# Optimization experiments

Hardware: AMD Instinct MI355X
Metric: run time of the kernel (lower is better)

The kernel has to match this reference:

```python
import jax, jax.numpy as jnp
import numpy as np

M = 15
WIN = 5  # tension detector window_size
SIGMA = 0.1
_ZETA = np.array([14.134725, 21.02204, 25.010858, 30.424876, 32.935062,
                  37.586178, 40.91872, 43.327073, 48.005151, 49.773832,
                  52.970321, 56.446248, 59.347044, 60.831779, 65.112544], dtype=np.float32)
GAMMAS = jnp.asarray(_ZETA)                       # [M]
PHI = jnp.asarray(np.exp(-SIGMA * np.abs(_ZETA)).astype(np.float32))  # [M]

B, S, I, H = 256, 512, 256, 512


def setup_inputs() -> dict:
    key = jax.random.key(0)
    ks = jax.random.split(key, 12)
    s_i = 1.0 / np.sqrt(I)
    s_h = 1.0 / np.sqrt(H)
    return {
        "x": jax.random.normal(ks[0], (B, S, I), dtype=jnp.float32),
        # LSTMCell params (PyTorch layout: gates i,f,g,o)
        "W_ih": jax.random.normal(ks[1], (4 * H, I), dtype=jnp.float32) * s_i,
        "W_hh": jax.random.normal(ks[2], (4 * H, H), dtype=jnp.float32) * s_h,
        "b_ih": jax.random.normal(ks[3], (4 * H,), dtype=jnp.float32) * s_h,
        "b_hh": jax.random.normal(ks[4], (4 * H,), dtype=jnp.float32) * s_h,
        # spectrum analyzer input_proj: Linear(I -> 2M)
        "W_proj": jax.random.normal(ks[5], (2 * M, I), dtype=jnp.float32) * s_i,
        "b_proj": jax.random.normal(ks[6], (2 * M,), dtype=jnp.float32) * s_i,
        # tension detector change_detector: Linear(2H->H), ReLU, Linear(H->1), Sigmoid
        "W_t1": jax.random.normal(ks[7], (H, 2 * H), dtype=jnp.float32) * (1.0 / np.sqrt(2 * H)),
        "b_t1": jax.random.normal(ks[8], (H,), dtype=jnp.float32) * s_h,
        "W_t2": jax.random.normal(ks[9], (1, H), dtype=jnp.float32) * s_h,
        "b_t2": jax.random.normal(ks[10], (1,), dtype=jnp.float32) * s_h,
        # zeta memory gate_combiner: Linear(2 -> 1)
        "W_g": jax.random.normal(ks[11], (1, 2), dtype=jnp.float32) * 0.5,
        "b_g": jnp.zeros((1,), dtype=jnp.float32),
    }


def _forward(x, W_ih, W_hh, b_ih, b_hh, W_proj, b_proj, W_t1, b_t1, W_t2, b_t2, W_g, b_g):
    batch = x.shape[0]
    seq_len = x.shape[1]
    hid = W_hh.shape[1]

    h0 = jnp.zeros((batch, hid), dtype=x.dtype)
    c0 = jnp.zeros((batch, hid), dtype=x.dtype)
    hist0 = jnp.zeros((batch, WIN, hid), dtype=x.dtype)

    def step(carry, inp):
        h, c, hist = carry
        x_t, t = inp                      # x_t: [B, I], t: scalar int
        tf = t.astype(x.dtype)

        # LSTMCell (produces h_new, c_new)
        gates = x_t @ W_ih.T + b_ih + h @ W_hh.T + b_hh   # [B, 4H]
        gi, gf, gg, go = jnp.split(gates, 4, axis=1)
        c_new = jax.nn.sigmoid(gf) * c + jax.nn.sigmoid(gi) * jnp.tanh(gg)
        h_new = jax.nn.sigmoid(go) * jnp.tanh(c_new)

        # ZetaSpectrumAnalyzer on x_t
        proj = x_t @ W_proj.T + b_proj                     # [B, 2M]
        cos_coeffs, sin_coeffs = proj[:, :M], proj[:, M:]
        zc = jnp.cos(GAMMAS * tf)                          # [M]
        zs = jnp.sin(GAMMAS * tf)
        cos_corr = jnp.sum(cos_coeffs * zc * PHI, axis=1)
        sin_corr = jnp.sum(sin_coeffs * zs * PHI, axis=1)
        resonance = jax.nn.sigmoid(jnp.sqrt(cos_corr**2 + sin_corr**2 + 1e-8) - 0.5)[:, None]  # [B,1]

        # TensionMarkerDetector on OLD h (history stores detached old h)
        hist = hist.at[:, t % WIN].set(jax.lax.stop_gradient(h))
        h_mean = hist.mean(axis=1)                         # [B, H]
        comp = jnp.concatenate([h, h_mean], axis=1)        # [B, 2H]
        tension = jax.nn.sigmoid(jax.nn.relu(comp @ W_t1.T + b_t1) @ W_t2.T + b_t2)  # [B,1]
        tension = jnp.where(t < 2, jnp.zeros_like(tension), tension)

        # ZetaMemoryGated on OLD h
        zeta_weight = jnp.sum(PHI * jnp.cos(GAMMAS * tf)) / M  # scalar
        m_raw = zeta_weight * h                                # [B, H]
        gate_in = jnp.concatenate([resonance, tension], axis=1)  # [B, 2]
        gate = jax.nn.sigmoid(gate_in @ W_g.T + b_g)             # [B, 1]
        h_out = h_new + gate * m_raw

        return (h_out, c_new, hist), h_out

    xs = (jnp.swapaxes(x, 0, 1), jnp.arange(seq_len, dtype=jnp.int32))
    (h_n, c_n, _), ys = jax.lax.scan(step, (h0, c0, hist0), xs)
    output = jnp.swapaxes(ys, 0, 1)        # [B, S, H]
    return output, h_n[None], c_n[None]


def reference(x, W_ih, W_hh, b_ih, b_hh, W_proj, b_proj, W_t1, b_t1, W_t2, b_t2, W_g, b_g):
    return _forward(x, W_ih, W_hh, b_ih, b_hh, W_proj, b_proj, W_t1, b_t1, W_t2, b_t2, W_g, b_g)
```

## Files before the change

### kernel.cpp

```cpp
#include <hip/hip_runtime.h>

typedef _Float16 f16;
typedef _Float16 f16x8 __attribute__((ext_vector_type(8)));
typedef float f32x4 __attribute__((ext_vector_type(4)));
typedef float f32x2 __attribute__((ext_vector_type(2)));
typedef unsigned long long u64;

#define DEVFN static __device__ __forceinline__

#define NBLK 256

#define OFF_WCAT 0ULL
#define OFF_WT1A (OFF_WCAT + 2048ULL*768*2)
#define OFF_WT1B (OFF_WT1A + 512ULL*512*2)
#define OFF_HB0  (OFF_WT1B + 512ULL*512*2)
#define OFF_HB1  (OFF_HB0  + 256ULL*512*2)
#define OFF_XB0  (OFF_HB1  + 256ULL*512*2)
#define OFF_XB1  (OFF_XB0  + 256ULL*256*2)
#define OFF_XB2  (OFF_XB1  + 256ULL*256*2)
#define OFF_BSUM (OFF_XB2  + 256ULL*256*2)
#define OFF_U    (OFF_BSUM + 2048ULL*4)
#define OFF_V    (OFF_U    + 512ULL*256*4)
#define OFF_CU   (OFF_V    + 512ULL*256*4)
#define OFF_CV   (OFF_CU   + 512ULL*4)
#define OFF_ZETA (OFF_CV   + 512ULL*4)
#define OFF_RES  (OFF_ZETA + 512ULL*4)
#define OFF_TENSP (OFF_RES + 512ULL*256*4)
#define OFF_SLOT (OFF_TENSP + 16384ULL*4)

__constant__ float CGAM[15] = {14.134725f, 21.02204f, 25.010858f, 30.424876f, 32.935062f,
  37.586178f, 40.91872f, 43.327073f, 48.005151f, 49.773832f, 52.970321f,
  56.446248f, 59.347044f, 60.831779f, 65.112544f};

DEVFN float sigf(float v) { return 1.f / (1.f + __expf(-v)); }
DEVFN float tanh_(float v) {
  v = fminf(fmaxf(v, -15.f), 15.f);
  float e = __expf(2.f * v);
  return (e - 1.f) / (e + 1.f);
}

DEVFN float ald_f32(const float* p) {
  unsigned v = __hip_atomic_load((const unsigned*)p, __ATOMIC_RELAXED, __HIP_MEMORY_SCOPE_AGENT);
  union { unsigned u; float f; } c; c.u = v; return c.f;
}
DEVFN void ast_f32(float* p, float v) {
  union { float f; unsigned u; } c; c.f = v;
  __hip_atomic_store((unsigned*)p, c.u, __ATOMIC_RELAXED, __HIP_MEMORY_SCOPE_AGENT);
}
DEVFN u64 ald_u64(const void* p) {
  return __hip_atomic_load((const u64*)p, __ATOMIC_RELAXED, __HIP_MEMORY_SCOPE_AGENT);
}
DEVFN void ast_u32(void* p, unsigned v) {
  __hip_atomic_store((unsigned*)p, v, __ATOMIC_RELAXED, __HIP_MEMORY_SCOPE_AGENT);
}

DEVFN void post(unsigned* slot, unsigned v) {
  asm volatile("s_waitcnt vmcnt(0)" ::: "memory");
  __syncthreads();
  if (threadIdx.x == 0)
    __hip_atomic_store(slot, v, __ATOMIC_RELAXED, __HIP_MEMORY_SCOPE_AGENT);
}
DEVFN void wait_line(const unsigned* line, unsigned target) {
  if (threadIdx.x < 64) {
    const unsigned* pp = line + (threadIdx.x & 31);
    long sp = 0;
    for (;;) {
      unsigned v = __hip_atomic_load(pp, __ATOMIC_RELAXED, __HIP_MEMORY_SCOPE_AGENT);
      if (__all(v >= target)) break;
      __builtin_amdgcn_s_sleep(1);
      if (++sp > (1L << 21)) break;
    }
  }
  __syncthreads();
}

__global__ void k_init(const float* __restrict__ x, const float* __restrict__ Wih,
                       const float* __restrict__ Whh, const float* __restrict__ bih,
                       const float* __restrict__ bhh, const float* __restrict__ Wt1f,
                       char* __restrict__ ws) {
  f16* Wcat = (f16*)(ws + OFF_WCAT);
  f16* WhmA = (f16*)(ws + OFF_WT1A);
  f16* WmB  = (f16*)(ws + OFF_WT1B);
  f16* hb0  = (f16*)(ws + OFF_HB0);
  f16* xb0  = (f16*)(ws + OFF_XB0);
  f16* xb1  = (f16*)(ws + OFF_XB1);
  float* bsum = (float*)(ws + OFF_BSUM);
  float* tensP = (float*)(ws + OFF_TENSP);
  unsigned* slots = (unsigned*)(ws + OFF_SLOT);
  int gtid = blockIdx.x * blockDim.x + threadIdx.x;
  int nth = gridDim.x * blockDim.x;
  for (int i = gtid; i < 2048 * 768; i += nth) {
    int n = i / 768, k = i - n * 768;
    float w = (k < 256) ? Wih[n * 256 + k] : Whh[n * 512 + (k - 256)];
    Wcat[i] = (f16)w;
  }
  for (int i = gtid; i < 512 * 512; i += nth) {
    int n = i >> 9, k = i & 511;
    float wh = Wt1f[n * 1024 + k];
    float wm = Wt1f[n * 1024 + 512 + k] * 0.2f;
    WhmA[i] = (f16)(wh + wm);
    WmB[i]  = (f16)wm;
  }
  for (int i = gtid; i < 2048; i += nth) bsum[i] = bih[i] + bhh[i];
  for (int i = gtid; i < 256 * 512; i += nth) hb0[i] = (f16)0.f;
  for (int i = gtid; i < 256 * 256; i += nth) {
    int b = i >> 8, k = i & 255;
    xb0[i] = (f16)x[(size_t)b * 131072 + k];
    xb1[i] = (f16)x[(size_t)b * 131072 + 256 + k];
  }
  for (int i = gtid; i < 16384; i += nth) tensP[i] = 0.f;
  for (int i = gtid; i < 8 * 64; i += nth) slots[i] = 0u;
}

__global__ void k_tables(const float* __restrict__ Wproj, const float* __restrict__ bproj,
                         char* __restrict__ ws) {
  float* u    = (float*)(ws + OFF_U);
  float* v    = (float*)(ws + OFF_V);
  float* cu   = (float*)(ws + OFF_CU);
  float* cv   = (float*)(ws + OFF_CV);
  float* zeta = (float*)(ws + OFF_ZETA);
  int t = blockIdx.x;
  int k = threadIdx.x;
  float tf = (float)t;
  float cg[15], sg[15], ph[15];
  #pragma unroll
  for (int m = 0; m < 15; ++m) {
    float ang = CGAM[m] * tf;
    cg[m] = cosf(ang);
    sg[m] = sinf(ang);
    ph[m] = (float)exp(-0.1 * (double)CGAM[m]);
  }
  float uu = 0.f, vv = 0.f;
  #pragma unroll
  for (int m = 0; m < 15; ++m) {
    uu += Wproj[m * 256 + k] * cg[m] * ph[m];
    vv += Wproj[(15 + m) * 256 + k] * sg[m] * ph[m];
  }
  u[t * 256 + k] = uu;
  v[t * 256 + k] = vv;
  if (k == 0) {
    float a = 0.f, b2 = 0.f, z = 0.f;
    #pragma unroll
    for (int m = 0; m < 15; ++m) {
      a  += bproj[m] * cg[m] * ph[m];
      b2 += bproj[15 + m] * sg[m] * ph[m];
      z  += ph[m] * cg[m];
    }
    cu[t] = a; cv[t] = b2; zeta[t] = z / 15.f;
  }
}

__global__ void k_res(const float* __restrict__ x, char* __restrict__ ws) {
  const float* u  = (const float*)(ws + OFF_U);
  const float* v  = (const float*)(ws + OFF_V);
  const float* cu = (const float*)(ws + OFF_CU);
  const float* cv = (const float*)(ws + OFF_CV);
  float* resb     = (float*)(ws + OFF_RES);
  int wid = blockIdx.x * 4 + (threadIdx.x >> 6);
  int l = threadIdx.x & 63;
  int b = wid >> 9, t = wid & 511;
  const f32x4 xx = *(const f32x4*)(x + ((size_t)(b * 512 + t)) * 256 + l * 4);
  const f32x4 uu = *(const f32x4*)(u + t * 256 + l * 4);
  const f32x4 vv = *(const f32x4*)(v + t * 256 + l * 4);
  float cc = xx[0]*uu[0] + xx[1]*uu[1] + xx[2]*uu[2] + xx[3]*uu[3];
  float ss = xx[0]*vv[0] + xx[1]*vv[1] + xx[2]*vv[2] + xx[3]*vv[3];
  #pragma unroll
  for (int m = 1; m < 64; m <<= 1) { cc += __shfl_xor(cc, m); ss += __shfl_xor(ss, m); }
  if (l == 0) {
    cc += cu[t]; ss += cv[t];
    float r = sqrtf(cc * cc + ss * ss + 1e-8f) - 0.5f;
    resb[t * 256 + b] = sigf(r);
  }
}

#define MFMA16(qv, wv, av) av = __builtin_amdgcn_mfma_f32_16x16x32_f16(qv, wv, av, 0, 0, 0)

__global__ void __launch_bounds__(256, 1)
k_lstm(const float* __restrict__ x, const float* __restrict__ bt1,
       const float* __restrict__ wt2, const float* __restrict__ bt2,
       const float* __restrict__ wg, const float* __restrict__ bg,
       float* __restrict__ out, char* __restrict__ ws) {
  extern __shared__ char lds[];
  char*  sH  = lds;
  char*  sXt = lds + 32768;
  float* sT  = (float*)(lds + 49152);
  float* sX  = (float*)(lds + 58368);
  float* sGZ = (float*)(lds + 68608);

  const f16* __restrict__ Wcat = (const f16*)(ws + OFF_WCAT);
  const f16* __restrict__ WhmA = (const f16*)(ws + OFF_WT1A);
  const f16* __restrict__ WmB  = (const f16*)(ws + OFF_WT1B);
  f16* hb[2] = { (f16*)(ws + OFF_HB0), (f16*)(ws + OFF_HB1) };
  f16* xb[3] = { (f16*)(ws + OFF_XB0), (f16*)(ws + OFF_XB1), (f16*)(ws + OFF_XB2) };
  const float* bsum = (const float*)(ws + OFF_BSUM);
  const float* zeta = (const float*)(ws + OFF_ZETA);
  const float* resb = (const float*)(ws + OFF_RES);
  float* tensP = (float*)(ws + OFF_TENSP);
  unsigned* slots = (unsigned*)(ws + OFF_SLOT);

  const int tid = threadIdx.x;
  const int w = tid >> 6, l = tid & 63;
  const int r0 = l & 15, kq = l >> 4;
  const int bid = blockIdx.x;
  const int p = bid >> 5, q = bid & 31;
  const int c0 = q * 16, m0 = p * 32;

  unsigned* slotH = slots + p * 64;
  unsigned* myH = slotH + q;

  f16x8 wbh[16], wbx[8];
  {
    const f16* Wr = Wcat + (size_t)(w * 512 + c0 + r0) * 768 + kq * 8;
    #pragma unroll
    for (int ks = 0; ks < 16; ++ks) wbh[ks] = *(const f16x8*)(Wr + 256 + ks * 32);
    #pragma unroll
    for (int ks = 0; ks < 8; ++ks)  wbx[ks] = *(const f16x8*)(Wr + ks * 32);
  }
  f16x8 wbhm[4], wbm[4];
  {
    const f16* Wa = WhmA + (size_t)(q * 16 + r0) * 512 + w * 128 + kq * 8;
    const f16* Wb = WmB  + (size_t)(q * 16 + r0) * 512 + w * 128 + kq * 8;
    #pragma unroll
    for (int ks = 0; ks < 4; ++ks) {
      wbhm[ks] = *(const f16x8*)(Wa + ks * 32);
      wbm[ks]  = *(const f16x8*)(Wb + ks * 32);
    }
  }
  const float b1a = bt1[q * 16 + r0], w2a = wt2[q * 16 + r0];

  const int b_loc = tid >> 3, c_loc = (tid & 7) * 2;
  const int pb = m0 + b_loc;
  float bsv[4][2];
  #pragma unroll
  for (int g = 0; g < 4; ++g) {
    bsv[g][0] = bsum[g * 512 + c0 + c_loc];
    bsv[g][1] = bsum[g * 512 + c0 + c_loc + 1];
  }
  const float wg0 = wg[0], wg1 = wg[1], bt2v = bt2[0], bgv = bg[0];
  float cst[2] = {0.f, 0.f};
  float hst[2] = {0.f, 0.f};
  float hnp[2] = {0.f, 0.f};

  f32x4 gho0 = {0,0,0,0}, gho1 = {0,0,0,0};
  f32x4 t1o0 = {0,0,0,0}, t1o1 = {0,0,0,0};
  f32x4 R[4][2];
  #pragma unroll
  for (int s = 0; s < 4; ++s) { R[s][0] = (f32x4){0,0,0,0}; R[s][1] = (f32x4){0,0,0,0}; }

  f32x4 ppx0 = {0,0,0,0}, ppx1 = {0,0,0,0};
  {
    u64 xlo[4], xhi[4];
    #pragma unroll
    for (int i = 0; i < 4; ++i) {
      const int B = i * 256 + tid;
      const int row = B >> 5, c = B & 31;
      const u64* pp = (const u64*)(xb[0] + (size_t)(m0 + row) * 256 + c * 8);
      xlo[i] = ald_u64(pp); xhi[i] = ald_u64(pp + 1);
    }
    #pragma unroll
    for (int i = 0; i < 4; ++i) {
      const int B = i * 256 + tid;
      const int row = B >> 5, c = B & 31;
      union { u64 qq[2]; uint4 v4; } uq; uq.qq[0] = xlo[i]; uq.qq[1] = xhi[i];
      *(uint4*)(sXt + row * 512 + ((c ^ (row & 7)) << 4)) = uq.v4;
    }
    __syncthreads();
    #pragma unroll
    for (int ks = 0; ks < 8; ++ks) {
      const int cc = (((ks * 4 + kq) ^ (r0 & 7)) << 4);
      f16x8 a0 = *(const f16x8*)(sXt + r0 * 512 + cc);
      f16x8 a1 = *(const f16x8*)(sXt + (r0 + 16) * 512 + cc);
      MFMA16(a0, wbx[ks], ppx0); MFMA16(a1, wbx[ks], ppx1);
    }
    __syncthreads();
  }

  for (int t = 0; t < 512; ++t) {
    wait_line(slotH, (unsigned)t);

    {
      float tn = 0.f;
      if (t >= 3) {
        const float* tpb = tensP + ((size_t)((t - 1) & 1) * 8 + p) * 1024;
        const int s8 = tid & 7;
        float acc = 0.f;
        #pragma unroll
        for (int j2 = 0; j2 < 4; ++j2)
          acc += ald_f32(tpb + (s8 * 4 + j2) * 32 + b_loc);
        acc += __shfl_xor(acc, 1); acc += __shfl_xor(acc, 2); acc += __shfl_xor(acc, 4);
        tn = sigf(acc + bt2v);
      }
      float g = 0.f;
      if (t >= 1) {
        float rs = resb[(t - 1) * 256 + pb];
        g = sigf(wg0 * rs + wg1 * tn + bgv) * zeta[t - 1];
      }
      if ((tid & 7) == 0) sGZ[b_loc] = g;
    }

    f32x2 xv = {0.f, 0.f};
    if (tid >= 128 && t < 510)
      xv = *(const f32x2*)(x + ((size_t)(m0 + q) * 512 + (t + 2)) * 256 + (tid - 128) * 2);
    if (t > 0) {
      const f16* hsrc = hb[(t - 1) & 1];
      u64 lo[8], hi[8];
      #pragma unroll
      for (int i = 0; i < 8; ++i) {
        const int B = i * 256 + tid;
        const int row = B >> 6, c = B & 63;
        const u64* pp = (const u64*)(hsrc + (size_t)(m0 + row) * 512 + c * 8);
        lo[i] = ald_u64(pp); hi[i] = ald_u64(pp + 1);
      }
      #pragma unroll
      for (int i = 0; i < 8; ++i) {
        const int B = i * 256 + tid;
        const int row = B >> 6, c = B & 63;
        union { u64 qq[2]; uint4 v4; } uq; uq.qq[0] = lo[i]; uq.qq[1] = hi[i];
        *(uint4*)(sH + row * 1024 + ((c ^ (row & 7)) << 4)) = uq.v4;
      }
    }
    if (t < 511) {
      const f16* xsrc = xb[(t + 1) % 3];
      u64 xlo[4], xhi[4];
      #pragma unroll
      for (int i = 0; i < 4; ++i) {
        const int B = i * 256 + tid;
        const int row = B >> 5, c = B & 31;
        const u64* pp = (const u64*)(xsrc + (size_t)(m0 + row) * 256 + c * 8);
        xlo[i] = ald_u64(pp); xhi[i] = ald_u64(pp + 1);
      }
      #pragma unroll
      for (int i = 0; i < 4; ++i) {
        const int B = i * 256 + tid;
        const int row = B >> 5, c = B & 31;
        union { u64 qq[2]; uint4 v4; } uq; uq.qq[0] = xlo[i]; uq.qq[1] = xhi[i];
        *(uint4*)(sXt + row * 512 + ((c ^ (row & 7)) << 4)) = uq.v4;
      }
    }
    __syncthreads();

    f32x4 ghn0 = {0,0,0,0}, ghn1 = {0,0,0,0};
    f32x4 t1n0 = {0,0,0,0}, t1n1 = {0,0,0,0};
    f32x4 cnw0 = {0,0,0,0}, cnw1 = {0,0,0,0};
    if (t > 0) {
      #pragma unroll
      for (int ks = 0; ks < 16; ++ks) {
        const int cc = (((ks * 4 + kq) ^ (r0 & 7)) << 4);
        f16x8 q0 = *(const f16x8*)(sH + r0 * 1024 + cc);
        f16x8 q1 = *(const f16x8*)(sH + (r0 + 16) * 1024 + cc);
        MFMA16(q0, wbh[ks], ghn0); MFMA16(q1, wbh[ks], ghn1);
      }
      #pragma unroll
      for (int ks = 0; ks < 4; ++ks) {
        const int cc = ((((w * 4 + ks) * 4 + kq) ^ (r0 & 7)) << 4);
        f16x8 q0 = *(const f16x8*)(sH + r0 * 1024 + cc);
        f16x8 q1 = *(const f16x8*)(sH + (r0 + 16) * 1024 + cc);
        MFMA16(q0, wbhm[ks], t1n0); MFMA16(q1, wbhm[ks], t1n1);
        MFMA16(q0, wbm[ks],  cnw0); MFMA16(q1, wbm[ks],  cnw1);
      }
    }

    {
      float gz0[4], gz1[4];
      #pragma unroll
      for (int r = 0; r < 4; ++r) { gz0[r] = sGZ[kq * 4 + r]; gz1[r] = sGZ[16 + kq * 4 + r]; }
      f32x4 co0, co1, tp0, tp1;
      #pragma unroll
      for (int r = 0; r < 4; ++r) {
        gho0[r] = ghn0[r] + gz0[r] * gho0[r];
        gho1[r] = ghn1[r] + gz1[r] * gho1[r];
        t1o0[r] = t1n0[r] + gz0[r] * t1o0[r];
        t1o1[r] = t1n1[r] + gz1[r] * t1o1[r];
        co0[r] = cnw0[r] + gz0[r] * R[0][0][r];
        co1[r] = cnw1[r] + gz1[r] * R[0][1][r];
        tp0[r] = t1o0[r] + R[0][0][r] + R[1][0][r] + R[2][0][r] + R[3][0][r];
        tp1[r] = t1o1[r] + R[0][1][r] + R[1][1][r] + R[2][1][r] + R[3][1][r];
      }
      #pragma unroll
      for (int s = 3; s > 0; --s) { R[s][0] = R[s - 1][0]; R[s][1] = R[s - 1][1]; }
      R[0][0] = co0; R[0][1] = co1;
      const int rb = kq * 4;
      float* tpx = sT + w * 576 + l * 9;
      #pragma unroll
      for (int r = 0; r < 4; ++r) {
        sX[(w * 32 + rb + r) * 20 + r0]      = ppx0[r] + gho0[r];
        sX[(w * 32 + 16 + rb + r) * 20 + r0] = ppx1[r] + gho1[r];
        tpx[r] = tp0[r]; tpx[4 + r] = tp1[r];
      }
    }
    __syncthreads();

    if (w == 0) {
      float sr0[4], sr1[4];
      #pragma unroll
      for (int r = 0; r < 4; ++r) {
        const float* t0 = sT + l * 9;
        float p0 = t0[r] + t0[576 + r] + t0[1152 + r] + t0[1728 + r] + b1a;
        float p1 = t0[4 + r] + t0[576 + 4 + r] + t0[1152 + 4 + r] + t0[1728 + 4 + r] + b1a;
        sr0[r] = fmaxf(p0, 0.f) * w2a;
        sr1[r] = fmaxf(p1, 0.f) * w2a;
      }
      #pragma unroll
      for (int m = 1; m < 16; m <<= 1) {
        #pragma unroll
        for (int r = 0; r < 4; ++r) { sr0[r] += __shfl_xor(sr0[r], m); sr1[r] += __shfl_xor(sr1[r], m); }
      }
      if (r0 == 0) {
        float* tp = tensP + (((size_t)(t & 1) * 8 + p) * 32 + q) * 32 + kq * 4;
        #pragma unroll
        for (int r = 0; r < 4; ++r) { ast_f32(tp + r, sr0[r]); ast_f32(tp + 16 + r, sr1[r]); }
      }
    }

    float hn_[2];
    #pragma unroll
    for (int e = 0; e < 2; ++e) {
      float gi = sX[(      b_loc) * 20 + c_loc + e] + bsv[0][e];
      float gf = sX[( 32 + b_loc) * 20 + c_loc + e] + bsv[1][e];
      float gg = sX[( 64 + b_loc) * 20 + c_loc + e] + bsv[2][e];
      float go = sX[( 96 + b_loc) * 20 + c_loc + e] + bsv[3][e];
      float c_new = sigf(gf) * cst[e] + sigf(gi) * tanh_(gg);
      cst[e] = c_new;
      hn_[e] = sigf(go) * tanh_(c_new);
    }
    float gzb = sGZ[b_loc];
    float hop[2] = { hnp[0] + gzb * hst[0], hnp[1] + gzb * hst[1] };
    {
      union { f16 h2[2]; unsigned u; } ph_;
      ph_.h2[0] = (f16)hn_[0]; ph_.h2[1] = (f16)hn_[1];
      ast_u32(hb[t & 1] + (size_t)pb * 512 + c0 + c_loc, ph_.u);
    }
    if (tid >= 128 && t < 510) {
      union { f16 h2[2]; unsigned u; } px;
      px.h2[0] = (f16)xv[0]; px.h2[1] = (f16)xv[1];
      ast_u32(xb[(t + 2) % 3] + (size_t)(m0 + q) * 256 + (tid - 128) * 2, px.u);
    }
    post(myH, (unsigned)(t + 1));

    if (t >= 1) {
      f32x2 ov = {hop[0], hop[1]};
      *(f32x2*)(out + ((size_t)pb * 512 + (t - 1)) * 512 + c0 + c_loc) = ov;
    }
    hst[0] = hop[0]; hst[1] = hop[1];
    hnp[0] = hn_[0]; hnp[1] = hn_[1];
    if (t < 511) {
      ppx0 = (f32x4){0,0,0,0}; ppx1 = (f32x4){0,0,0,0};
      #pragma unroll
      for (int ks = 0; ks < 8; ++ks) {
        const int cc = (((ks * 4 + kq) ^ (r0 & 7)) << 4);
        f16x8 a0 = *(const f16x8*)(sXt + r0 * 512 + cc);
        f16x8 a1 = *(const f16x8*)(sXt + (r0 + 16) * 512 + cc);
        MFMA16(a0, wbx[ks], ppx0); MFMA16(a1, wbx[ks], ppx1);
      }
    }
  }

  wait_line(slotH, 512u);
  {
    const float* tpb = tensP + ((size_t)(511 & 1) * 8 + p) * 1024;
    const int s8 = tid & 7;
    float acc = 0.f;
    #pragma unroll
    for (int j2 = 0; j2 < 4; ++j2)
      acc += ald_f32(tpb + (s8 * 4 + j2) * 32 + b_loc);
    acc += __shfl_xor(acc, 1); acc += __shfl_xor(acc, 2); acc += __shfl_xor(acc, 4);
    float tn = sigf(acc + bt2v);
    float rs = resb[511 * 256 + pb];
    float gzb = sigf(wg0 * rs + wg1 * tn + bgv) * zeta[511];
    float hop[2] = { hnp[0] + gzb * hst[0], hnp[1] + gzb * hst[1] };
    f32x2 ov = {hop[0], hop[1]};
    *(f32x2*)(out + ((size_t)pb * 512 + 511) * 512 + c0 + c_loc) = ov;
    *(f32x2*)(out + 67108864 + (size_t)pb * 512 + c0 + c_loc) = ov;
    f32x2 cv2 = {cst[0], cst[1]};
    *(f32x2*)(out + 67108864 + 131072 + (size_t)pb * 512 + c0 + c_loc) = cv2;
  }
}

extern "C" void kernel_launch(void* const* d_in, const int* in_sizes, int n_in,
                              void* d_out, int out_size, void* d_ws, size_t ws_size,
                              hipStream_t stream) {
  (void)in_sizes; (void)n_in; (void)out_size; (void)ws_size;
  const float* x     = (const float*)d_in[0];
  const float* Wih   = (const float*)d_in[1];
  const float* Whh   = (const float*)d_in[2];
  const float* bih   = (const float*)d_in[3];
  const float* bhh   = (const float*)d_in[4];
  const float* Wproj = (const float*)d_in[5];
  const float* bproj = (const float*)d_in[6];
  const float* Wt1   = (const float*)d_in[7];
  const float* bt1   = (const float*)d_in[8];
  const float* Wt2   = (const float*)d_in[9];
  const float* bt2   = (const float*)d_in[10];
  const float* Wg    = (const float*)d_in[11];
  const float* bg    = (const float*)d_in[12];
  float* out = (float*)d_out;
  char* ws = (char*)d_ws;
  hipFuncSetAttribute((const void*)k_lstm, hipFuncAttributeMaxDynamicSharedMemorySize, 131072);
  k_init<<<dim3(1024), dim3(256), 0, stream>>>(x, Wih, Whh, bih, bhh, Wt1, ws);
  k_tables<<<dim3(512), dim3(256), 0, stream>>>(Wproj, bproj, ws);
  k_res<<<dim3(32768), dim3(256), 0, stream>>>(x, ws);
  k_lstm<<<dim3(NBLK), dim3(256), 68736, stream>>>(x, bt1, Wt2, bt2, Wg, bg, out, ws);
}
```

Measured before the change: 3.514 ms.

## Replace per-step block flag barrier with tagged data words for fine-grained sync

Removes the per-block slot post/wait barrier and instead packs a step tag next to each published h value and tension partial in 64-bit words. Consumers spin on the tags of exactly the data they need, which drops the global vmcnt drain and syncthreads from the post path. The x input is now read directly from fp32 global memory and converted in-kernel instead of going through shared f16 staging buffers. The trade-off is double the bytes per published value and more polling traffic, plus an added syncthreads in the x staging path.

After: 4.050 ms. +15.2%, slower.

```diff
diff --git a/kernel.cpp b/kernel.cpp
--- a/kernel.cpp
+++ b/kernel.cpp
@@ -13,20 +13,15 @@
 #define OFF_WCAT 0ULL
 #define OFF_WT1A (OFF_WCAT + 2048ULL*768*2)
 #define OFF_WT1B (OFF_WT1A + 512ULL*512*2)
-#define OFF_HB0  (OFF_WT1B + 512ULL*512*2)
-#define OFF_HB1  (OFF_HB0  + 256ULL*512*2)
-#define OFF_XB0  (OFF_HB1  + 256ULL*512*2)
-#define OFF_XB1  (OFF_XB0  + 256ULL*256*2)
-#define OFF_XB2  (OFF_XB1  + 256ULL*256*2)
-#define OFF_BSUM (OFF_XB2  + 256ULL*256*2)
+#define OFF_HBT  (OFF_WT1B + 512ULL*512*2)
+#define OFF_TT   (OFF_HBT  + 2ULL*256*256*8)
+#define OFF_BSUM (OFF_TT   + 2ULL*8192*8)
 #define OFF_U    (OFF_BSUM + 2048ULL*4)
 #define OFF_V    (OFF_U    + 512ULL*256*4)
 #define OFF_CU   (OFF_V    + 512ULL*256*4)
 #define OFF_CV   (OFF_CU   + 512ULL*4)
 #define OFF_ZETA (OFF_CV   + 512ULL*4)
 #define OFF_RES  (OFF_ZETA + 512ULL*4)
-#define OFF_TENSP (OFF_RES + 512ULL*256*4)
-#define OFF_SLOT (OFF_TENSP + 16384ULL*4)
 
 __constant__ float CGAM[15] = {14.134725f, 21.02204f, 25.010858f, 30.424876f, 32.935062f,
   37.586178f, 40.91872f, 43.327073f, 48.005151f, 49.773832f, 52.970321f,
@@ -39,39 +34,11 @@
   return (e - 1.f) / (e + 1.f);
 }
 
-DEVFN float ald_f32(const float* p) {
-  unsigned v = __hip_atomic_load((const unsigned*)p, __ATOMIC_RELAXED, __HIP_MEMORY_SCOPE_AGENT);
-  union { unsigned u; float f; } c; c.u = v; return c.f;
-}
-DEVFN void ast_f32(float* p, float v) {
-  union { float f; unsigned u; } c; c.f = v;
-  __hip_atomic_store((unsigned*)p, c.u, __ATOMIC_RELAXED, __HIP_MEMORY_SCOPE_AGENT);
-}
 DEVFN u64 ald_u64(const void* p) {
   return __hip_atomic_load((const u64*)p, __ATOMIC_RELAXED, __HIP_MEMORY_SCOPE_AGENT);
 }
-DEVFN void ast_u32(void* p, unsigned v) {
-  __hip_atomic_store((unsigned*)p, v, __ATOMIC_RELAXED, __HIP_MEMORY_SCOPE_AGENT);
-}
-
-DEVFN void post(unsigned* slot, unsigned v) {
-  asm volatile("s_waitcnt vmcnt(0)" ::: "memory");
-  __syncthreads();
-  if (threadIdx.x == 0)
-    __hip_atomic_store(slot, v, __ATOMIC_RELAXED, __HIP_MEMORY_SCOPE_AGENT);
-}
-DEVFN void wait_line(const unsigned* line, unsigned target) {
-  if (threadIdx.x < 64) {
-    const unsigned* pp = line + (threadIdx.x & 31);
-    long sp = 0;
-    for (;;) {
-      unsigned v = __hip_atomic_load(pp, __ATOMIC_RELAXED, __HIP_MEMORY_SCOPE_AGENT);
-      if (__all(v >= target)) break;
-      __builtin_amdgcn_s_sleep(1);
-      if (++sp > (1L << 21)) break;
-    }
-  }
-  __syncthreads();
+DEVFN void ast_u64(void* p, u64 v) {
+  __hip_atomic_store((u64*)p, v, __ATOMIC_RELAXED, __HIP_MEMORY_SCOPE_AGENT);
 }
 
 __global__ void k_init(const float* __restrict__ x, const float* __restrict__ Wih,
@@ -81,12 +48,9 @@
   f16* Wcat = (f16*)(ws + OFF_WCAT);
   f16* WhmA = (f16*)(ws + OFF_WT1A);
   f16* WmB  = (f16*)(ws + OFF_WT1B);
-  f16* hb0  = (f16*)(ws + OFF_HB0);
-  f16* xb0  = (f16*)(ws + OFF_XB0);
-  f16* xb1  = (f16*)(ws + OFF_XB1);
+  u64* hbT  = (u64*)(ws + OFF_HBT);
+  u64* tT   = (u64*)(ws + OFF_TT);
   float* bsum = (float*)(ws + OFF_BSUM);
-  float* tensP = (float*)(ws + OFF_TENSP);
-  unsigned* slots = (unsigned*)(ws + OFF_SLOT);
   int gtid = blockIdx.x * blockDim.x + threadIdx.x;
   int nth = gridDim.x * blockDim.x;
   for (int i = gtid; i < 2048 * 768; i += nth) {
@@ -102,14 +66,8 @@
     WmB[i]  = (f16)wm;
   }
   for (int i = gtid; i < 2048; i += nth) bsum[i] = bih[i] + bhh[i];
-  for (int i = gtid; i < 256 * 512; i += nth) hb0[i] = (f16)0.f;
-  for (int i = gtid; i < 256 * 256; i += nth) {
-    int b = i >> 8, k = i & 255;
-    xb0[i] = (f16)x[(size_t)b * 131072 + k];
-    xb1[i] = (f16)x[(size_t)b * 131072 + 256 + k];
-  }
-  for (int i = gtid; i < 16384; i += nth) tensP[i] = 0.f;
-  for (int i = gtid; i < 8 * 64; i += nth) slots[i] = 0u;
+  for (int i = gtid; i < 2 * 256 * 256; i += nth) hbT[i] = 0ull;
+  for (int i = gtid; i < 2 * 8192; i += nth) tT[i] = 0ull;
 }
 
 __global__ void k_tables(const float* __restrict__ Wproj, const float* __restrict__ bproj,
@@ -190,13 +148,11 @@
   const f16* __restrict__ Wcat = (const f16*)(ws + OFF_WCAT);
   const f16* __restrict__ WhmA = (const f16*)(ws + OFF_WT1A);
   const f16* __restrict__ WmB  = (const f16*)(ws + OFF_WT1B);
-  f16* hb[2] = { (f16*)(ws + OFF_HB0), (f16*)(ws + OFF_HB1) };
-  f16* xb[3] = { (f16*)(ws + OFF_XB0), (f16*)(ws + OFF_XB1), (f16*)(ws + OFF_XB2) };
+  u64* hbT = (u64*)(ws + OFF_HBT);
+  u64* tT  = (u64*)(ws + OFF_TT);
   const float* bsum = (const float*)(ws + OFF_BSUM);
   const float* zeta = (const float*)(ws + OFF_ZETA);
   const float* resb = (const float*)(ws + OFF_RES);
-  float* tensP = (float*)(ws + OFF_TENSP);
-  unsigned* slots = (unsigned*)(ws + OFF_SLOT);
 
   const int tid = threadIdx.x;
   const int w = tid >> 6, l = tid & 63;
@@ -204,9 +160,6 @@
   const int bid = blockIdx.x;
   const int p = bid >> 5, q = bid & 31;
   const int c0 = q * 16, m0 = p * 32;
-
-  unsigned* slotH = slots + p * 64;
-  unsigned* myH = slotH + q;
 
   f16x8 wbh[16], wbx[8];
   {
@@ -249,20 +202,17 @@
 
   f32x4 ppx0 = {0,0,0,0}, ppx1 = {0,0,0,0};
   {
-    u64 xlo[4], xhi[4];
     #pragma unroll
     for (int i = 0; i < 4; ++i) {
-      const int B = i * 256 + tid;
-      const int row = B >> 5, c = B & 31;
-      const u64* pp = (const u64*)(xb[0] + (size_t)(m0 + row) * 256 + c * 8);
-      xlo[i] = ald_u64(pp); xhi[i] = ald_u64(pp + 1);
-    }
-    #pragma unroll
-    for (int i = 0; i < 4; ++i) {
-      const int B = i * 256 + tid;
-      const int row = B >> 5, c = B & 31;
-      union { u64 qq[2]; uint4 v4; } uq; uq.qq[0] = xlo[i]; uq.qq[1] = xhi[i];
-      *(uint4*)(sXt + row * 512 + ((c ^ (row & 7)) << 4)) = uq.v4;
+      const int U = i * 256 + tid;
+      const int row = U >> 5, c = U & 31;
+      const float* xp = x + ((size_t)(m0 + row) * 512 + 0) * 256 + c * 8;
+      f32x4 xa = *(const f32x4*)xp;
+      f32x4 xb_ = *(const f32x4*)(xp + 4);
+      f16x8 xf;
+      #pragma unroll
+      for (int r = 0; r < 4; ++r) { xf[r] = (f16)xa[r]; xf[4 + r] = (f16)xb_[r]; }
+      *(f16x8*)(sXt + row * 512 + ((c ^ (row & 7)) << 4)) = xf;
     }
     __syncthreads();
     #pragma unroll
@@ -276,17 +226,31 @@
   }
 
   for (int t = 0; t < 512; ++t) {
-    wait_line(slotH, (unsigned)t);
+    const int par = t & 1, parm = (t - 1) & 1;
 
     {
       float tn = 0.f;
       if (t >= 3) {
-        const float* tpb = tensP + ((size_t)((t - 1) & 1) * 8 + p) * 1024;
-        const int s8 = tid & 7;
+        const u64* tpb = tT + ((size_t)parm * 8 + p) * 1024 + (size_t)(tid & 7) * 128 + b_loc;
+        u64 v[4];
+        long sp = 0;
+        for (;;) {
+          bool ok = true;
+          #pragma unroll
+          for (int j2 = 0; j2 < 4; ++j2) {
+            v[j2] = ald_u64(tpb + j2 * 32);
+            ok &= ((unsigned)v[j2] == (unsigned)t);
+          }
+          if (ok) break;
+          __builtin_amdgcn_s_sleep(1);
+          if (++sp > (1L << 20)) break;
+        }
         float acc = 0.f;
         #pragma unroll
-        for (int j2 = 0; j2 < 4; ++j2)
-          acc += ald_f32(tpb + (s8 * 4 + j2) * 32 + b_loc);
+        for (int j2 = 0; j2 < 4; ++j2) {
+          union { unsigned u; float f; } c2; c2.u = (unsigned)(v[j2] >> 32);
+          acc += c2.f;
+        }
         acc += __shfl_xor(acc, 1); acc += __shfl_xor(acc, 2); acc += __shfl_xor(acc, 4);
         tn = sigf(acc + bt2v);
       }
@@ -295,46 +259,32 @@
         float rs = resb[(t - 1) * 256 + pb];
         g = sigf(wg0 * rs + wg1 * tn + bgv) * zeta[t - 1];
       }
-      if ((tid & 7) == 0) sGZ[b_loc] = g;
-    }
-
-    f32x2 xv = {0.f, 0.f};
-    if (tid >= 128 && t < 510)
-      xv = *(const f32x2*)(x + ((size_t)(m0 + q) * 512 + (t + 2)) * 256 + (tid - 128) * 2);
+      if ((tid & 7) == 0) sGZ[par * 32 + b_loc] = g;
+    }
+
     if (t > 0) {
-      const f16* hsrc = hb[(t - 1) & 1];
-      u64 lo[8], hi[8];
-      #pragma unroll
-      for (int i = 0; i < 8; ++i) {
-        const int B = i * 256 + tid;
-        const int row = B >> 6, c = B & 63;
-        const u64* pp = (const u64*)(hsrc + (size_t)(m0 + row) * 512 + c * 8);
-        lo[i] = ald_u64(pp); hi[i] = ald_u64(pp + 1);
-      }
-      #pragma unroll
-      for (int i = 0; i < 8; ++i) {
-        const int B = i * 256 + tid;
-        const int row = B >> 6, c = B & 63;
-        union { u64 qq[2]; uint4 v4; } uq; uq.qq[0] = lo[i]; uq.qq[1] = hi[i];
-        *(uint4*)(sH + row * 1024 + ((c ^ (row & 7)) << 4)) = uq.v4;
-      }
-    }
-    if (t < 511) {
-      const f16* xsrc = xb[(t + 1) % 3];
-      u64 xlo[4], xhi[4];
-      #pragma unroll
-      for (int i = 0; i < 4; ++i) {
-        const int B = i * 256 + tid;
-        const int row = B >> 5, c = B & 31;
-        const u64* pp = (const u64*)(xsrc + (size_t)(m0 + row) * 256 + c * 8);
-        xlo[i] = ald_u64(pp); xhi[i] = ald_u64(pp + 1);
-      }
-      #pragma unroll
-      for (int i = 0; i < 4; ++i) {
-        const int B = i * 256 + tid;
-        const int row = B >> 5, c = B & 31;
-        union { u64 qq[2]; uint4 v4; } uq; uq.qq[0] = xlo[i]; uq.qq[1] = xhi[i];
-        *(uint4*)(sXt + row * 512 + ((c ^ (row & 7)) << 4)) = uq.v4;
+      const u64* hsrc = hbT + (size_t)parm * 65536 + (size_t)m0 * 256;
+      const unsigned want = (unsigned)t;
+      unsigned done = 0;
+      long sp = 0;
+      for (;;) {
+        #pragma unroll
+        for (int j = 0; j < 8; ++j) if (!(done & (1u << j))) {
+          const int P = j * 256 + tid;
+          const int row = P >> 6, c = P & 63;
+          const u64* pp = hsrc + (size_t)row * 256 + (size_t)c * 4;
+          u64 q0 = ald_u64(pp), q1 = ald_u64(pp + 1), q2 = ald_u64(pp + 2), q3 = ald_u64(pp + 3);
+          if (((unsigned)q0 == want) & ((unsigned)q1 == want) &
+              ((unsigned)q2 == want) & ((unsigned)q3 == want)) {
+            uint4 d = { (unsigned)(q0 >> 32), (unsigned)(q1 >> 32),
+                        (unsigned)(q2 >> 32), (unsigned)(q3 >> 32) };
+            *(uint4*)(sH + row * 1024 + ((c ^ (row & 7)) << 4)) = d;
+            done |= 1u << j;
+          }
+        }
+        if (done == 0xffu) break;
+        __builtin_amdgcn_s_sleep(1);
+        if (++sp > (1L << 20)) break;
       }
     }
     __syncthreads();
@@ -363,7 +313,10 @@
     {
       float gz0[4], gz1[4];
       #pragma unroll
-      for (int r = 0; r < 4; ++r) { gz0[r] = sGZ[kq * 4 + r]; gz1[r] = sGZ[16 + kq * 4 + r]; }
+      for (int r = 0; r < 4; ++r) {
+        gz0[r] = sGZ[par * 32 + kq * 4 + r];
+        gz1[r] = sGZ[par * 32 + 16 + kq * 4 + r];
+      }
       f32x4 co0, co1, tp0, tp1;
       #pragma unroll
       for (int r = 0; r < 4; ++r) {
@@ -390,6 +343,18 @@
     }
     __syncthreads();
 
+    f32x4 xr[8];
+    if (t < 511) {
+      #pragma unroll
+      for (int i = 0; i < 4; ++i) {
+        const int U = i * 256 + tid;
+        const int row = U >> 5, c = U & 31;
+        const float* xp = x + ((size_t)(m0 + row) * 512 + (t + 1)) * 256 + c * 8;
+        xr[2 * i]     = *(const f32x4*)xp;
+        xr[2 * i + 1] = *(const f32x4*)(xp + 4);
+      }
+    }
+
     if (w == 0) {
       float sr0[4], sr1[4];
       #pragma unroll
@@ -406,9 +371,14 @@
         for (int r = 0; r < 4; ++r) { sr0[r] += __shfl_xor(sr0[r], m); sr1[r] += __shfl_xor(sr1[r], m); }
       }
       if (r0 == 0) {
-        float* tp = tensP + (((size_t)(t & 1) * 8 + p) * 32 + q) * 32 + kq * 4;
+        u64* tp = tT + ((size_t)par * 8 + p) * 1024 + (size_t)q * 32 + kq * 4;
+        const u64 tag = (u64)(unsigned)(t + 1);
         #pragma unroll
-        for (int r = 0; r < 4; ++r) { ast_f32(tp + r, sr0[r]); ast_f32(tp + 16 + r, sr1[r]); }
+        for (int r = 0; r < 4; ++r) {
+          union { float f; unsigned u; } a0, a1; a0.f = sr0[r]; a1.f = sr1[r];
+          ast_u64(tp + r,      tag | ((u64)a0.u << 32));
+          ast_u64(tp + 16 + r, tag | ((u64)a1.u << 32));
+        }
       }
     }
 
@@ -423,19 +393,15 @@
       cst[e] = c_new;
       hn_[e] = sigf(go) * tanh_(c_new);
     }
-    float gzb = sGZ[b_loc];
+    float gzb = sGZ[par * 32 + b_loc];
     float hop[2] = { hnp[0] + gzb * hst[0], hnp[1] + gzb * hst[1] };
+
     {
       union { f16 h2[2]; unsigned u; } ph_;
       ph_.h2[0] = (f16)hn_[0]; ph_.h2[1] = (f16)hn_[1];
-      ast_u32(hb[t & 1] + (size_t)pb * 512 + c0 + c_loc, ph_.u);
-    }
-    if (tid >= 128 && t < 510) {
-      union { f16 h2[2]; unsigned u; } px;
-      px.h2[0] = (f16)xv[0]; px.h2[1] = (f16)xv[1];
-      ast_u32(xb[(t + 2) % 3] + (size_t)(m0 + q) * 256 + (tid - 128) * 2, px.u);
-    }
-    post(myH, (unsigned)(t + 1));
+      u64 v = (u64)(unsigned)(t + 1) | ((u64)ph_.u << 32);
+      ast_u64(hbT + (size_t)par * 65536 + (size_t)pb * 256 + q * 8 + (tid & 7), v);
+    }
 
     if (t >= 1) {
       f32x2 ov = {hop[0], hop[1]};
@@ -444,6 +410,16 @@
     hst[0] = hop[0]; hst[1] = hop[1];
     hnp[0] = hn_[0]; hnp[1] = hn_[1];
     if (t < 511) {
+      #pragma unroll
+      for (int i = 0; i < 4; ++i) {
+        const int U = i * 256 + tid;
+        const int row = U >> 5, c = U & 31;
+        f16x8 xf;
+        #pragma unroll
+        for (int r = 0; r < 4; ++r) { xf[r] = (f16)xr[2 * i][r]; xf[4 + r] = (f16)xr[2 * i + 1][r]; }
+        *(f16x8*)(sXt + row * 512 + ((c ^ (row & 7)) << 4)) = xf;
+      }
+      __syncthreads();
       ppx0 = (f32x4){0,0,0,0}; ppx1 = (f32x4){0,0,0,0};
       #pragma unroll
       for (int ks = 0; ks < 8; ++ks) {
@@ -455,14 +431,27 @@
     }
   }
 
-  wait_line(slotH, 512u);
   {
-    const float* tpb = tensP + ((size_t)(511 & 1) * 8 + p) * 1024;
-    const int s8 = tid & 7;
+    const u64* tpb = tT + ((size_t)(511 & 1) * 8 + p) * 1024 + (size_t)(tid & 7) * 128 + b_loc;
+    u64 v[4];
+    long sp = 0;
+    for (;;) {
+      bool ok = true;
+      #pragma unroll
+      for (int j2 = 0; j2 < 4; ++j2) {
+        v[j2] = ald_u64(tpb + j2 * 32);
+        ok &= ((unsigned)v[j2] == 512u);
+      }
+      if (ok) break;
+      __builtin_amdgcn_s_sleep(1);
+      if (++sp > (1L << 20)) break;
+    }
     float acc = 0.f;
     #pragma unroll
-    for (int j2 = 0; j2 < 4; ++j2)
-      acc += ald_f32(tpb + (s8 * 4 + j2) * 32 + b_loc);
+    for (int j2 = 0; j2 < 4; ++j2) {
+      union { unsigned u; float f; } c2; c2.u = (unsigned)(v[j2] >> 32);
+      acc += c2.f;
+    }
     acc += __shfl_xor(acc, 1); acc += __shfl_xor(acc, 2); acc += __shfl_xor(acc, 4);
     float tn = sigf(acc + bt2v);
     float rs = resb[511 * 256 + pb];
@@ -499,5 +488,5 @@
   k_init<<<dim3(1024), dim3(256), 0, stream>>>(x, Wih, Whh, bih, bhh, Wt1, ws);
   k_tables<<<dim3(512), dim3(256), 0, stream>>>(Wproj, bproj, ws);
   k_res<<<dim3(32768), dim3(256), 0, stream>>>(x, ws);
-  k_lstm<<<dim3(NBLK), dim3(256), 68736, stream>>>(x, bt1, Wt2, bt2, Wg, bg, out, ws);
-}
+  k_lstm<<<dim3(NBLK), dim3(256), 68864, stream>>>(x, bt1, Wt2, bt2, Wg, bg, out, ws);
+}
```

## Stream x directly into double-buffered LDS instead of global fp16 ring

Applied to the files above, without the earlier changes.

Removes the global fp16 x ring buffer (xb0..2), in which each block converted and stored part of the next step's input for other blocks. Instead, each block loads its own fp32 x rows for step t+2 straight from the input, converts them to fp16, and writes them into one of two alternating LDS tiles after the current step's input MFMA. This removes a global round-trip and the cross-block dependency on x from the per-step critical path, at the cost of more LDS and more fp32 global reads per block. The tension reduction is also spread across all four waves instead of only wave 0.

After: 3.552 ms. About the same (+1.1%).

```diff
diff --git a/kernel.cpp b/kernel.cpp
--- a/kernel.cpp
+++ b/kernel.cpp
@@ -15,10 +15,7 @@
 #define OFF_WT1B (OFF_WT1A + 512ULL*512*2)
 #define OFF_HB0  (OFF_WT1B + 512ULL*512*2)
 #define OFF_HB1  (OFF_HB0  + 256ULL*512*2)
-#define OFF_XB0  (OFF_HB1  + 256ULL*512*2)
-#define OFF_XB1  (OFF_XB0  + 256ULL*256*2)
-#define OFF_XB2  (OFF_XB1  + 256ULL*256*2)
-#define OFF_BSUM (OFF_XB2  + 256ULL*256*2)
+#define OFF_BSUM (OFF_HB1  + 256ULL*512*2)
 #define OFF_U    (OFF_BSUM + 2048ULL*4)
 #define OFF_V    (OFF_U    + 512ULL*256*4)
 #define OFF_CU   (OFF_V    + 512ULL*256*4)
@@ -82,8 +79,6 @@
   f16* WhmA = (f16*)(ws + OFF_WT1A);
   f16* WmB  = (f16*)(ws + OFF_WT1B);
   f16* hb0  = (f16*)(ws + OFF_HB0);
-  f16* xb0  = (f16*)(ws + OFF_XB0);
-  f16* xb1  = (f16*)(ws + OFF_XB1);
   float* bsum = (float*)(ws + OFF_BSUM);
   float* tensP = (float*)(ws + OFF_TENSP);
   unsigned* slots = (unsigned*)(ws + OFF_SLOT);
@@ -103,11 +98,6 @@
   }
   for (int i = gtid; i < 2048; i += nth) bsum[i] = bih[i] + bhh[i];
   for (int i = gtid; i < 256 * 512; i += nth) hb0[i] = (f16)0.f;
-  for (int i = gtid; i < 256 * 256; i += nth) {
-    int b = i >> 8, k = i & 255;
-    xb0[i] = (f16)x[(size_t)b * 131072 + k];
-    xb1[i] = (f16)x[(size_t)b * 131072 + 256 + k];
-  }
   for (int i = gtid; i < 16384; i += nth) tensP[i] = 0.f;
   for (int i = gtid; i < 8 * 64; i += nth) slots[i] = 0u;
 }
@@ -181,17 +171,17 @@
        const float* __restrict__ wg, const float* __restrict__ bg,
        float* __restrict__ out, char* __restrict__ ws) {
   extern __shared__ char lds[];
-  char*  sH  = lds;
-  char*  sXt = lds + 32768;
-  float* sT  = (float*)(lds + 49152);
-  float* sX  = (float*)(lds + 58368);
-  float* sGZ = (float*)(lds + 68608);
+  char*  sH   = lds;
+  char*  sXt0 = lds + 32768;
+  char*  sXt1 = lds + 49152;
+  float* sT   = (float*)(lds + 65536);
+  float* sX   = (float*)(lds + 74752);
+  float* sGZ  = (float*)(lds + 84992);
 
   const f16* __restrict__ Wcat = (const f16*)(ws + OFF_WCAT);
   const f16* __restrict__ WhmA = (const f16*)(ws + OFF_WT1A);
   const f16* __restrict__ WmB  = (const f16*)(ws + OFF_WT1B);
   f16* hb[2] = { (f16*)(ws + OFF_HB0), (f16*)(ws + OFF_HB1) };
-  f16* xb[3] = { (f16*)(ws + OFF_XB0), (f16*)(ws + OFF_XB1), (f16*)(ws + OFF_XB2) };
   const float* bsum = (const float*)(ws + OFF_BSUM);
   const float* zeta = (const float*)(ws + OFF_ZETA);
   const float* resb = (const float*)(ws + OFF_RES);
@@ -249,39 +239,50 @@
 
   f32x4 ppx0 = {0,0,0,0}, ppx1 = {0,0,0,0};
   {
-    u64 xlo[4], xhi[4];
     #pragma unroll
     for (int i = 0; i < 4; ++i) {
-      const int B = i * 256 + tid;
-      const int row = B >> 5, c = B & 31;
-      const u64* pp = (const u64*)(xb[0] + (size_t)(m0 + row) * 256 + c * 8);
-      xlo[i] = ald_u64(pp); xhi[i] = ald_u64(pp + 1);
-    }
-    #pragma unroll
-    for (int i = 0; i < 4; ++i) {
-      const int B = i * 256 + tid;
-      const int row = B >> 5, c = B & 31;
-      union { u64 qq[2]; uint4 v4; } uq; uq.qq[0] = xlo[i]; uq.qq[1] = xhi[i];
-      *(uint4*)(sXt + row * 512 + ((c ^ (row & 7)) << 4)) = uq.v4;
+      const int U = i * 256 + tid;
+      const int row = U >> 5, c = U & 31;
+      const float* xp = x + ((size_t)(m0 + row) * 512 + 0) * 256 + c * 8;
+      f32x4 xa = *(const f32x4*)xp;
+      f32x4 xb_ = *(const f32x4*)(xp + 4);
+      f16x8 xf;
+      #pragma unroll
+      for (int r = 0; r < 4; ++r) { xf[r] = (f16)xa[r]; xf[4 + r] = (f16)xb_[r]; }
+      *(f16x8*)(sXt0 + row * 512 + ((c ^ (row & 7)) << 4)) = xf;
     }
     __syncthreads();
     #pragma unroll
     for (int ks = 0; ks < 8; ++ks) {
       const int cc = (((ks * 4 + kq) ^ (r0 & 7)) << 4);
-      f16x8 a0 = *(const f16x8*)(sXt + r0 * 512 + cc);
-      f16x8 a1 = *(const f16x8*)(sXt + (r0 + 16) * 512 + cc);
+      f16x8 a0 = *(const f16x8*)(sXt0 + r0 * 512 + cc);
+      f16x8 a1 = *(const f16x8*)(sXt0 + (r0 + 16) * 512 + cc);
       MFMA16(a0, wbx[ks], ppx0); MFMA16(a1, wbx[ks], ppx1);
     }
+    #pragma unroll
+    for (int i = 0; i < 4; ++i) {
+      const int U = i * 256 + tid;
+      const int row = U >> 5, c = U & 31;
+      const float* xp = x + ((size_t)(m0 + row) * 512 + 1) * 256 + c * 8;
+      f32x4 xa = *(const f32x4*)xp;
+      f32x4 xb_ = *(const f32x4*)(xp + 4);
+      f16x8 xf;
+      #pragma unroll
+      for (int r = 0; r < 4; ++r) { xf[r] = (f16)xa[r]; xf[4 + r] = (f16)xb_[r]; }
+      *(f16x8*)(sXt1 + row * 512 + ((c ^ (row & 7)) << 4)) = xf;
+    }
     __syncthreads();
   }
 
   for (int t = 0; t < 512; ++t) {
+    const int par = t & 1, parm = (t - 1) & 1;
+
     wait_line(slotH, (unsigned)t);
 
     {
       float tn = 0.f;
       if (t >= 3) {
-        const float* tpb = tensP + ((size_t)((t - 1) & 1) * 8 + p) * 1024;
+        const float* tpb = tensP + ((size_t)parm * 8 + p) * 1024;
         const int s8 = tid & 7;
         float acc = 0.f;
         #pragma unroll
@@ -298,11 +299,8 @@
       if ((tid & 7) == 0) sGZ[b_loc] = g;
     }
 
-    f32x2 xv = {0.f, 0.f};
-    if (tid >= 128 && t < 510)
-      xv = *(const f32x2*)(x + ((size_t)(m0 + q) * 512 + (t + 2)) * 256 + (tid - 128) * 2);
     if (t > 0) {
-      const f16* hsrc = hb[(t - 1) & 1];
+      const f16* hsrc = hb[parm];
       u64 lo[8], hi[8];
       #pragma unroll
       for (int i = 0; i < 8; ++i) {
@@ -317,24 +315,6 @@
         const int row = B >> 6, c = B & 63;
         union { u64 qq[2]; uint4 v4; } uq; uq.qq[0] = lo[i]; uq.qq[1] = hi[i];
         *(uint4*)(sH + row * 1024 + ((c ^ (row & 7)) << 4)) = uq.v4;
-      }
-    }
-    if (t < 511) {
-      const f16* xsrc = xb[(t + 1) % 3];
-      u64 xlo[4], xhi[4];
-      #pragma unroll
-      for (int i = 0; i < 4; ++i) {
-        const int B = i * 256 + tid;
-        const int row = B >> 5, c = B & 31;
-        const u64* pp = (const u64*)(xsrc + (size_t)(m0 + row) * 256 + c * 8);
-        xlo[i] = ald_u64(pp); xhi[i] = ald_u64(pp + 1);
-      }
-      #pragma unroll
-      for (int i = 0; i < 4; ++i) {
-        const int B = i * 256 + tid;
-        const int row = B >> 5, c = B & 31;
-        union { u64 qq[2]; uint4 v4; } uq; uq.qq[0] = xlo[i]; uq.qq[1] = xhi[i];
-        *(uint4*)(sXt + row * 512 + ((c ^ (row & 7)) << 4)) = uq.v4;
       }
     }
     __syncthreads();
@@ -390,25 +370,20 @@
     }
     __syncthreads();
 
-    if (w == 0) {
-      float sr0[4], sr1[4];
-      #pragma unroll
-      for (int r = 0; r < 4; ++r) {
-        const float* t0 = sT + l * 9;
-        float p0 = t0[r] + t0[576 + r] + t0[1152 + r] + t0[1728 + r] + b1a;
-        float p1 = t0[4 + r] + t0[576 + 4 + r] + t0[1152 + 4 + r] + t0[1728 + 4 + r] + b1a;
-        sr0[r] = fmaxf(p0, 0.f) * w2a;
-        sr1[r] = fmaxf(p1, 0.f) * w2a;
-      }
-      #pragma unroll
-      for (int m = 1; m < 16; m <<= 1) {
-        #pragma unroll
-        for (int r = 0; r < 4; ++r) { sr0[r] += __shfl_xor(sr0[r], m); sr1[r] += __shfl_xor(sr1[r], m); }
-      }
-      if (r0 == 0) {
-        float* tp = tensP + (((size_t)(t & 1) * 8 + p) * 32 + q) * 32 + kq * 4;
-        #pragma unroll
-        for (int r = 0; r < 4; ++r) { ast_f32(tp + r, sr0[r]); ast_f32(tp + 16 + r, sr1[r]); }
+    {
+      const int rf0 = w * 2;
+      #pragma unroll
+      for (int rr = 0; rr < 2; ++rr) {
+        const int rf = rf0 + rr;
+        float v = sT[l * 9 + rf] + sT[576 + l * 9 + rf]
+                + sT[1152 + l * 9 + rf] + sT[1728 + l * 9 + rf] + b1a;
+        float s = fmaxf(v, 0.f) * w2a;
+        s += __shfl_xor(s, 1); s += __shfl_xor(s, 2);
+        s += __shfl_xor(s, 4); s += __shfl_xor(s, 8);
+        if (r0 == 0) {
+          int row = (rf < 4) ? (kq * 4 + rf) : (16 + kq * 4 + (rf - 4));
+          ast_f32(tensP + (((size_t)par * 8 + p) * 32 + q) * 32 + row, s);
+        }
       }
     }
 
@@ -428,12 +403,7 @@
     {
       union { f16 h2[2]; unsigned u; } ph_;
       ph_.h2[0] = (f16)hn_[0]; ph_.h2[1] = (f16)hn_[1];
-      ast_u32(hb[t & 1] + (size_t)pb * 512 + c0 + c_loc, ph_.u);
-    }
-    if (tid >= 128 && t < 510) {
-      union { f16 h2[2]; unsigned u; } px;
-      px.h2[0] = (f16)xv[0]; px.h2[1] = (f16)xv[1];
-      ast_u32(xb[(t + 2) % 3] + (size_t)(m0 + q) * 256 + (tid - 128) * 2, px.u);
+      ast_u32(hb[par] + (size_t)pb * 512 + c0 + c_loc, ph_.u);
     }
     post(myH, (unsigned)(t + 1));
 
@@ -444,13 +414,29 @@
     hst[0] = hop[0]; hst[1] = hop[1];
     hnp[0] = hn_[0]; hnp[1] = hn_[1];
     if (t < 511) {
+      char* sXcur = (((t + 1) & 1) ? sXt1 : sXt0);
       ppx0 = (f32x4){0,0,0,0}; ppx1 = (f32x4){0,0,0,0};
       #pragma unroll
       for (int ks = 0; ks < 8; ++ks) {
         const int cc = (((ks * 4 + kq) ^ (r0 & 7)) << 4);
-        f16x8 a0 = *(const f16x8*)(sXt + r0 * 512 + cc);
-        f16x8 a1 = *(const f16x8*)(sXt + (r0 + 16) * 512 + cc);
+        f16x8 a0 = *(const f16x8*)(sXcur + r0 * 512 + cc);
+        f16x8 a1 = *(const f16x8*)(sXcur + (r0 + 16) * 512 + cc);
         MFMA16(a0, wbx[ks], ppx0); MFMA16(a1, wbx[ks], ppx1);
+      }
+      if (t < 510) {
+        char* sXnxt = ((t & 1) ? sXt1 : sXt0);
+        #pragma unroll
+        for (int i = 0; i < 4; ++i) {
+          const int U = i * 256 + tid;
+          const int row = U >> 5, c = U & 31;
+          const float* xp = x + ((size_t)(m0 + row) * 512 + (t + 2)) * 256 + c * 8;
+          f32x4 xa = *(const f32x4*)xp;
+          f32x4 xb_ = *(const f32x4*)(xp + 4);
+          f16x8 xf;
+          #pragma unroll
+          for (int r = 0; r < 4; ++r) { xf[r] = (f16)xa[r]; xf[4 + r] = (f16)xb_[r]; }
+          *(f16x8*)(sXnxt + row * 512 + ((c ^ (row & 7)) << 4)) = xf;
+        }
       }
     }
   }
@@ -499,5 +485,5 @@
   k_init<<<dim3(1024), dim3(256), 0, stream>>>(x, Wih, Whh, bih, bhh, Wt1, ws);
   k_tables<<<dim3(512), dim3(256), 0, stream>>>(Wproj, bproj, ws);
   k_res<<<dim3(32768), dim3(256), 0, stream>>>(x, ws);
-  k_lstm<<<dim3(NBLK), dim3(256), 68736, stream>>>(x, bt1, Wt2, bt2, Wg, bg, out, ws);
-}
+  k_lstm<<<dim3(NBLK), dim3(256), 85120, stream>>>(x, bt1, Wt2, bt2, Wg, bg, out, ws);
+}
```
